# Kernel tuning notes

Measured on AMD Instinct MI355X. Metric: run time of the kernel, lower is better.

The kernel has to match this reference:

```python
import jax, jax.numpy as jnp
import numpy as np

# fp4 e2m1 positive value grid and midpoints between adjacent grid values
_GRID = jnp.array([0.0, 0.5, 1.0, 1.5, 2.0, 3.0, 4.0, 6.0], dtype=jnp.float32)
_MIDS = jnp.array([0.25, 0.75, 1.25, 1.75, 2.5, 3.5, 5.0], dtype=jnp.float32)
BLOCK = 32               # MX block size
E8M0_BIAS = 127
F32_MIN_NORMAL = float(2.0 ** -126)
F4_E2M1_MAX_POW2 = 2     # log2 of largest power-of-two <= 6.0 -> 4.0


def _quantize_fp4(a):
    """Round-to-nearest-even onto the signed e2m1 grid."""
    mag = jnp.clip(jnp.abs(a), 0.0, 6.0)
    idx = jnp.searchsorted(_MIDS, mag, side='left')  # ties round down
    mids_pad = jnp.concatenate([_MIDS, jnp.array([-1.0], jnp.float32)])
    tie = mag == mids_pad[idx]
    idx = jnp.where(tie & (idx % 2 == 1), idx + 1, idx)  # ties-to-even mantissa
    return _GRID[idx] * jnp.where(a < 0, -1.0, 1.0)


def _floor_log2(m):
    """Exact floor(log2(m)) for m > 0, with corrections for fp rounding of log2."""
    e = jnp.floor(jnp.log2(m))
    e = jnp.where(jnp.exp2(e) > m, e - 1.0, e)
    e = jnp.where(jnp.exp2(e + 1.0) <= m, e + 1.0, e)
    return e


def _qdq_mxfp4(x):
    """Quantize-dequantize x to MX fp4_e2m1, block 32, FLOOR scale mode (to_mx + to_dtype)."""
    shp = x.shape
    xb = x.reshape(-1, BLOCK)
    max_abs = jnp.max(jnp.abs(xb), axis=1)
    eps = F32_MIN_NORMAL * (max_abs == 0).astype(jnp.float32)
    pow2 = _floor_log2(max_abs + eps)
    e_unb = jnp.clip(pow2 - F4_E2M1_MAX_POW2, -float(E8M0_BIAS), float(E8M0_BIAS) + 1.0)
    scale = jnp.maximum(jnp.exp2(e_unb), F32_MIN_NORMAL)  # [nblk]
    q = _quantize_fp4(xb / scale[:, None])
    return (q * scale[:, None]).reshape(shp)


def _dequant_weight(weight_packed, weight_scale, out_f, in_f):
    """Unpack uint8-packed fp4 (low nibble first), apply e8m0 block scales."""
    p = weight_packed.astype(jnp.int32)
    low = p & 0xF
    high = (p >> 4) & 0xF
    nib = jnp.stack([low, high], axis=-1).reshape(out_f, in_f)  # interleave low,high
    vals = _GRID[nib & 7] * jnp.where((nib & 8) > 0, -1.0, 1.0)
    s = jnp.exp2(weight_scale.astype(jnp.float32) - E8M0_BIAS)  # get_fp_scale(e8m0)
    return (vals.reshape(-1, BLOCK) * s[:, None]).reshape(out_f, in_f)


def setup_inputs() -> dict:
    key = jax.random.key(0)
    k1, k2, k3 = jax.random.split(key, 3)
    M, IN, OUT = 4096, 4096, 4096
    x = jax.random.normal(k1, (M, IN), dtype=jnp.float32)
    weight_packed = jax.random.randint(k2, (OUT, IN // 2), 0, 256, dtype=jnp.int32)
    weight_scale = jax.random.randint(k3, (OUT * IN // BLOCK,), 0, 135, dtype=jnp.int32)
    return {"x": x, "weight_packed": weight_packed, "weight_scale": weight_scale}


def reference(x, weight_packed, weight_scale):
    out_f = weight_packed.shape[0]
    in_f = weight_packed.shape[1] * 2
    xq = _qdq_mxfp4(x)                                       # qdq_mxfp4(x)
    w_dq = _dequant_weight(weight_packed, weight_scale, out_f, in_f)
    return xq @ w_dq.T                                       # matmul(x, w_dq.t())
```

## Files before the change

### kernel.cpp

```cpp
#include <hip/hip_runtime.h>
#include <stdint.h>

typedef __attribute__((ext_vector_type(4)))  int   intx4;
typedef __attribute__((ext_vector_type(8)))  int   intx8;
typedef __attribute__((ext_vector_type(16))) float floatx16;

#define GLL16(gp, lp)                                                               \
    __builtin_amdgcn_global_load_lds((const __attribute__((address_space(1))) unsigned int*)(gp), \
                                     (__attribute__((address_space(3))) unsigned int*)(lp), 16, 0, 0)
#define GLL4(gp, lp)                                                                \
    __builtin_amdgcn_global_load_lds((const __attribute__((address_space(1))) unsigned int*)(gp), \
                                     (__attribute__((address_space(3))) unsigned int*)(lp), 4, 0, 0)

__device__ __forceinline__ uint32_t enc1(float xv, float inv) {
    float a = fminf(fabsf(xv) * inv, 6.0f);
    int e;
    if (a < 2.0f)      e = (int)rintf(a + a);
    else if (a < 4.0f) e = (int)rintf(a) + 2;
    else               e = (int)rintf(a * 0.5f) + 4;
    return (uint32_t)e | ((__float_as_uint(xv) >> 28) & 8u);
}

__global__ __launch_bounds__(256) void quant_x_kernel(const float* __restrict__ x,
                                                      uint32_t* __restrict__ xq,
                                                      uint8_t* __restrict__ xs) {
    const int gl = blockIdx.x * 256 + threadIdx.x;
    const float4 v = ((const float4*)x)[gl];
    float m = fmaxf(fmaxf(fabsf(v.x), fabsf(v.y)), fmaxf(fabsf(v.z), fabsf(v.w)));
    m = fmaxf(m, __shfl_xor(m, 1));
    m = fmaxf(m, __shfl_xor(m, 2));
    m = fmaxf(m, __shfl_xor(m, 4));
    const unsigned ef = __float_as_uint(m) >> 23;
    const unsigned code = (ef < 3u) ? 1u : (ef - 2u);
    const float inv = __uint_as_float((254u - code) << 23);
    const uint32_t p = enc1(v.x, inv)        | (enc1(v.y, inv) << 4)
                     | (enc1(v.z, inv) << 8) | (enc1(v.w, inv) << 12);
    ((uint16_t*)xq)[gl] = (uint16_t)p;
    if ((gl & 7) == 0) xs[gl >> 3] = (uint8_t)code;
}

__global__ __launch_bounds__(256) void repack_kernel(const int* __restrict__ wp,
                                                     uint32_t* __restrict__ wrep,
                                                     int n4w,
                                                     const int* __restrict__ wsc,
                                                     uint32_t* __restrict__ ws,
                                                     int n4s) {
    const int t = blockIdx.x * 256 + threadIdx.x;
    if (t < n4w) {
        const int4 p = ((const int4*)wp)[t];
        wrep[t] = (uint32_t)(p.x & 0xFF) | ((uint32_t)(p.y & 0xFF) << 8)
                | ((uint32_t)(p.z & 0xFF) << 16) | ((uint32_t)(p.w & 0xFF) << 24);
    } else if (t - n4w < n4s) {
        const int i = t - n4w;
        const int4 p = ((const int4*)wsc)[i];
        ws[i] = (uint32_t)(p.x & 0xFF) | ((uint32_t)(p.y & 0xFF) << 8)
              | ((uint32_t)(p.z & 0xFF) << 16) | ((uint32_t)(p.w & 0xFF) << 24);
    }
}

__global__ __launch_bounds__(256) void tpose_s_kernel(const uint8_t* __restrict__ nat,
                                                      uint8_t* __restrict__ xs_t,
                                                      uint8_t* __restrict__ ws_t,
                                                      int R, int Ck) {
    __shared__ uint8_t raw[128 * 32];
    const int r0 = blockIdx.x * 128;
    const int c0 = blockIdx.y * 32;
    const int t = threadIdx.x;
    {
        const int r = t >> 1, hf = t & 1;
        const uint4 v = *(const uint4*)(nat + (size_t)(r0 + r) * Ck + c0 + hf * 16);
        *(uint4*)(raw + r * 32 + hf * 16) = v;
    }
    __syncthreads();
    const int c = t >> 3, q = t & 7;
    uint32_t d[4];
#pragma unroll
    for (int j = 0; j < 4; ++j) {
        const int mb = q * 16 + j * 4;
        d[j] = (uint32_t)raw[(mb + 0) * 32 + c]
             | ((uint32_t)raw[(mb + 1) * 32 + c] << 8)
             | ((uint32_t)raw[(mb + 2) * 32 + c] << 16)
             | ((uint32_t)raw[(mb + 3) * 32 + c] << 24);
    }
    uint8_t* outp = (r0 < R) ? (xs_t + (size_t)(c0 + c) * R + r0)
                             : (ws_t + (size_t)(c0 + c) * R + (r0 - R));
    *(uint4*)(outp + q * 16) = make_uint4(d[0], d[1], d[2], d[3]);
}

__global__ __launch_bounds__(256) void gemm_mx_kernel(const uint8_t* __restrict__ Apk,
                                                      const uint8_t* __restrict__ Bpk,
                                                      const uint8_t* __restrict__ AsT,
                                                      const uint8_t* __restrict__ BsT,
                                                      float* __restrict__ C,
                                                      int M, int N, int K) {
    __shared__ __align__(16) uint8_t sA[8192];
    __shared__ __align__(16) uint8_t sB[8192];
    __shared__ __align__(16) uint8_t sS[1024];

    const int tid = threadIdx.x;
    const int bm0 = blockIdx.y << 7;
    const int bn0 = blockIdx.x << 7;
    const int wave = tid >> 6;
    const int lane = tid & 63;
    const int wm = (wave >> 1) << 6;
    const int wn = (wave & 1) << 6;
    const int row = lane & 31;
    const int h = lane >> 5;
    const int Kb = K >> 1;

    const int s0 = tid, s1 = tid + 256;
    const int r0 = s0 >> 2, p0 = (s0 & 3) ^ ((r0 >> 1) & 3);
    const int r1 = s1 >> 2, p1 = (s1 & 3) ^ ((r1 >> 1) & 3);
    const uint8_t* Ag0 = Apk + (size_t)(bm0 + r0) * Kb + p0 * 16;
    const uint8_t* Ag1 = Apk + (size_t)(bm0 + r1) * Kb + p1 * 16;
    const uint8_t* Bg0 = Bpk + (size_t)(bn0 + r0) * Kb + p0 * 16;
    const uint8_t* Bg1 = Bpk + (size_t)(bn0 + r1) * Kb + p1 * 16;

    const int st = tid & 127;
    const int sj = st >> 5, si = st & 31;
    const uint8_t* Sg = (tid < 128) ? (AsT + (size_t)sj * M + bm0 + si * 4)
                                    : (BsT + (size_t)sj * N + bn0 + si * 4);
    uint8_t* Sl = sS + ((tid < 128) ? 0 : 512) + st * 4;
    const size_t sAdv = (size_t)4 * (size_t)((tid < 128) ? M : N);

    floatx16 acc[2][2];
#pragma unroll
    for (int a = 0; a < 2; ++a)
#pragma unroll
        for (int b = 0; b < 2; ++b)
#pragma unroll
            for (int r = 0; r < 16; ++r) acc[a][b][r] = 0.f;

    const int nchunk = K >> 7;
    const int ar0 = wm + row, ar1 = wm + 32 + row;
    const int br0 = wn + row, br1 = wn + 32 + row;

    for (int c = 0; c < nchunk; ++c) {
        __syncthreads();
        const size_t koff = (size_t)c << 6;
        GLL16(Ag0 + koff, sA + s0 * 16);
        GLL16(Ag1 + koff, sA + s1 * 16);
        GLL16(Bg0 + koff, sB + s0 * 16);
        GLL16(Bg1 + koff, sB + s1 * 16);
        GLL4(Sg + (size_t)c * sAdv, Sl);
        __syncthreads();

#pragma unroll
        for (int s = 0; s < 2; ++s) {
            const int kp = 2 * s + h;
            intx4 a4[2], b4[2];
            int sa[2], sb[2];
            a4[0] = *(const intx4*)(sA + ar0 * 64 + ((kp ^ ((ar0 >> 1) & 3)) << 4));
            a4[1] = *(const intx4*)(sA + ar1 * 64 + ((kp ^ ((ar1 >> 1) & 3)) << 4));
            b4[0] = *(const intx4*)(sB + br0 * 64 + ((kp ^ ((br0 >> 1) & 3)) << 4));
            b4[1] = *(const intx4*)(sB + br1 * 64 + ((kp ^ ((br1 >> 1) & 3)) << 4));
            sa[0] = sS[kp * 128 + ar0];
            sa[1] = sS[kp * 128 + ar1];
            sb[0] = sS[512 + kp * 128 + br0];
            sb[1] = sS[512 + kp * 128 + br1];
#pragma unroll
            for (int mt = 0; mt < 2; ++mt)
#pragma unroll
                for (int nt = 0; nt < 2; ++nt) {
                    intx8 a8 = {a4[mt][0], a4[mt][1], a4[mt][2], a4[mt][3], 0, 0, 0, 0};
                    intx8 b8 = {b4[nt][0], b4[nt][1], b4[nt][2], b4[nt][3], 0, 0, 0, 0};
                    acc[mt][nt] = __builtin_amdgcn_mfma_scale_f32_32x32x64_f8f6f4(
                        a8, b8, acc[mt][nt], 4, 4, 0, sa[mt], 0, sb[nt]);
                }
        }
    }

#pragma unroll
    for (int mt = 0; mt < 2; ++mt)
#pragma unroll
        for (int nt = 0; nt < 2; ++nt) {
            const int col = bn0 + wn + nt * 32 + row;
#pragma unroll
            for (int g = 0; g < 4; ++g) {
                const int rw = bm0 + wm + mt * 32 + 8 * g + 4 * h;
#pragma unroll
                for (int q = 0; q < 4; ++q)
                    C[(size_t)(rw + q) * N + col] = acc[mt][nt][4 * g + q];
            }
        }
}

extern "C" void kernel_launch(void* const* d_in, const int* in_sizes, int n_in,
                              void* d_out, int out_size, void* d_ws, size_t ws_size,
                              hipStream_t stream) {
    const float* x = (const float*)d_in[0];
    const int* wp = (const int*)d_in[1];
    const int* wsc = (const int*)d_in[2];
    float* out = (float*)d_out;

    const int K = 4096;
    const int M = in_sizes[0] / K;
    const int N = (in_sizes[1] * 2) / K;
    const int kbpr = K / 32;
    const int npack = N * K / 2;

    uint32_t* xq   = (uint32_t*)d_ws;
    uint8_t*  xs   = (uint8_t*)d_ws + (size_t)M * K / 2;
    uint8_t*  ws   = xs + (size_t)M * kbpr;
    uint32_t* wrep = (uint32_t*)(ws + (size_t)N * kbpr);
    uint8_t*  xs_t = (uint8_t*)(wrep + (size_t)npack / 4);
    uint8_t*  ws_t = xs_t + (size_t)M * kbpr;

    const int n4w = npack / 4;
    const int n4s = (N * kbpr) / 4;

    quant_x_kernel<<<(M * K / 4) / 256, 256, 0, stream>>>(x, xq, xs);
    repack_kernel<<<(n4w + n4s + 255) / 256, 256, 0, stream>>>(wp, wrep, n4w,
                                                               wsc, (uint32_t*)ws, n4s);
    dim3 tg(2 * M / 128, kbpr / 32);
    tpose_s_kernel<<<tg, 256, 0, stream>>>(xs, xs_t, ws_t, M, kbpr);

    dim3 grid(N / 128, M / 128);
    gemm_mx_kernel<<<grid, 256, 0, stream>>>((const uint8_t*)xq, (const uint8_t*)wrep,
                                             xs_t, ws_t, out, M, N, K);
}
```

Measured before the change: 193.0 us.

## Triple-buffer LDS tiles in MX GEMM with async prefetch two chunks ahead

Replaces the single-buffered load-sync-compute loop with a three-stage LDS ring where global_load_lds for chunk c+2 is issued before computing chunk c. Explicit vmcnt waits let outstanding loads overlap MFMA work, hiding global memory latency that previously stalled each iteration. This triples LDS use per block, which may cut occupancy, and relies on hand-counted vmcnt values being correct.

```diff
diff --git a/kernel.cpp b/kernel.cpp
--- a/kernel.cpp
+++ b/kernel.cpp
@@ -93,9 +93,9 @@
                                                       const uint8_t* __restrict__ BsT,
                                                       float* __restrict__ C,
                                                       int M, int N, int K) {
-    __shared__ __align__(16) uint8_t sA[8192];
-    __shared__ __align__(16) uint8_t sB[8192];
-    __shared__ __align__(16) uint8_t sS[1024];
+    __shared__ __align__(16) uint8_t sA[3][8192];
+    __shared__ __align__(16) uint8_t sB[3][8192];
+    __shared__ __align__(16) uint8_t sS[3][1024];
 
     const int tid = threadIdx.x;
     const int bm0 = blockIdx.y << 7;
@@ -120,7 +120,7 @@
     const int sj = st >> 5, si = st & 31;
     const uint8_t* Sg = (tid < 128) ? (AsT + (size_t)sj * M + bm0 + si * 4)
                                     : (BsT + (size_t)sj * N + bn0 + si * 4);
-    uint8_t* Sl = sS + ((tid < 128) ? 0 : 512) + st * 4;
+    const int sloff = ((tid < 128) ? 0 : 512) + st * 4;
     const size_t sAdv = (size_t)4 * (size_t)((tid < 128) ? M : N);
 
     floatx16 acc[2][2];
@@ -135,29 +135,32 @@
     const int ar0 = wm + row, ar1 = wm + 32 + row;
     const int br0 = wn + row, br1 = wn + 32 + row;
 
-    for (int c = 0; c < nchunk; ++c) {
-        __syncthreads();
+    auto STAGE = [&](int bf, int c) {
         const size_t koff = (size_t)c << 6;
-        GLL16(Ag0 + koff, sA + s0 * 16);
-        GLL16(Ag1 + koff, sA + s1 * 16);
-        GLL16(Bg0 + koff, sB + s0 * 16);
-        GLL16(Bg1 + koff, sB + s1 * 16);
-        GLL4(Sg + (size_t)c * sAdv, Sl);
-        __syncthreads();
-
+        GLL16(Ag0 + koff, &sA[bf][s0 * 16]);
+        GLL16(Ag1 + koff, &sA[bf][s1 * 16]);
+        GLL16(Bg0 + koff, &sB[bf][s0 * 16]);
+        GLL16(Bg1 + koff, &sB[bf][s1 * 16]);
+        GLL4(Sg + (size_t)c * sAdv, &sS[bf][sloff]);
+    };
+
+    auto COMPUTE = [&](int bf) {
+        const uint8_t* cA = sA[bf];
+        const uint8_t* cB = sB[bf];
+        const uint8_t* cS = sS[bf];
 #pragma unroll
         for (int s = 0; s < 2; ++s) {
             const int kp = 2 * s + h;
             intx4 a4[2], b4[2];
             int sa[2], sb[2];
-            a4[0] = *(const intx4*)(sA + ar0 * 64 + ((kp ^ ((ar0 >> 1) & 3)) << 4));
-            a4[1] = *(const intx4*)(sA + ar1 * 64 + ((kp ^ ((ar1 >> 1) & 3)) << 4));
-            b4[0] = *(const intx4*)(sB + br0 * 64 + ((kp ^ ((br0 >> 1) & 3)) << 4));
-            b4[1] = *(const intx4*)(sB + br1 * 64 + ((kp ^ ((br1 >> 1) & 3)) << 4));
-            sa[0] = sS[kp * 128 + ar0];
-            sa[1] = sS[kp * 128 + ar1];
-            sb[0] = sS[512 + kp * 128 + br0];
-            sb[1] = sS[512 + kp * 128 + br1];
+            a4[0] = *(const intx4*)(cA + ar0 * 64 + ((kp ^ ((ar0 >> 1) & 3)) << 4));
+            a4[1] = *(const intx4*)(cA + ar1 * 64 + ((kp ^ ((ar1 >> 1) & 3)) << 4));
+            b4[0] = *(const intx4*)(cB + br0 * 64 + ((kp ^ ((br0 >> 1) & 3)) << 4));
+            b4[1] = *(const intx4*)(cB + br1 * 64 + ((kp ^ ((br1 >> 1) & 3)) << 4));
+            sa[0] = cS[kp * 128 + ar0];
+            sa[1] = cS[kp * 128 + ar1];
+            sb[0] = cS[512 + kp * 128 + br0];
+            sb[1] = cS[512 + kp * 128 + br1];
 #pragma unroll
             for (int mt = 0; mt < 2; ++mt)
 #pragma unroll
@@ -168,6 +171,23 @@
                         a8, b8, acc[mt][nt], 4, 4, 0, sa[mt], 0, sb[nt]);
                 }
         }
+    };
+
+    STAGE(0, 0);
+    STAGE(1, 1);
+
+    int i0 = 0, i1 = 1, i2 = 2;
+    for (int c = 0; c < nchunk; ++c) {
+        __builtin_amdgcn_s_barrier();
+        asm volatile("" ::: "memory");
+        if (c + 2 < nchunk) STAGE(i2, c + 2);
+        if (c < nchunk - 2)      asm volatile("s_waitcnt vmcnt(10)" ::: "memory");
+        else if (c == nchunk - 2) asm volatile("s_waitcnt vmcnt(5)" ::: "memory");
+        else                      asm volatile("s_waitcnt vmcnt(0)" ::: "memory");
+        __builtin_amdgcn_s_barrier();
+        asm volatile("" ::: "memory");
+        COMPUTE(i0);
+        const int t = i0; i0 = i1; i1 = i2; i2 = t;
     }
 
 #pragma unroll
```

New measurement: 201.8 us. 1.05x slower.

## Double the K-chunk per iteration in MX fp4 GEMM with wider swizzle

Applied to the files above, without the earlier changes.

Each main-loop iteration of the GEMM now stages 256 K elements instead of 128, doubling the shared tiles for A, B and the scales and running four MFMA sub-steps per chunk. The LDS row stride grows to 128 bytes with an 8-way XOR swizzle to avoid bank conflicts. The aim is to halve the number of barrier pairs and make each load burst larger. The cost is doubled shared memory per block, which may lower occupancy, and there is still no double buffering.

```diff
diff --git a/kernel.cpp b/kernel.cpp
--- a/kernel.cpp
+++ b/kernel.cpp
@@ -93,9 +93,9 @@
                                                       const uint8_t* __restrict__ BsT,
                                                       float* __restrict__ C,
                                                       int M, int N, int K) {
-    __shared__ __align__(16) uint8_t sA[8192];
-    __shared__ __align__(16) uint8_t sB[8192];
-    __shared__ __align__(16) uint8_t sS[1024];
+    __shared__ __align__(16) uint8_t sA[16384];
+    __shared__ __align__(16) uint8_t sB[16384];
+    __shared__ __align__(16) uint8_t sS[2048];
 
     const int tid = threadIdx.x;
     const int bm0 = blockIdx.y << 7;
@@ -108,20 +108,25 @@
     const int h = lane >> 5;
     const int Kb = K >> 1;
 
-    const int s0 = tid, s1 = tid + 256;
-    const int r0 = s0 >> 2, p0 = (s0 & 3) ^ ((r0 >> 1) & 3);
-    const int r1 = s1 >> 2, p1 = (s1 & 3) ^ ((r1 >> 1) & 3);
-    const uint8_t* Ag0 = Apk + (size_t)(bm0 + r0) * Kb + p0 * 16;
-    const uint8_t* Ag1 = Apk + (size_t)(bm0 + r1) * Kb + p1 * 16;
-    const uint8_t* Bg0 = Bpk + (size_t)(bn0 + r0) * Kb + p0 * 16;
-    const uint8_t* Bg1 = Bpk + (size_t)(bn0 + r1) * Kb + p1 * 16;
+    const uint8_t* Ag[4];
+    const uint8_t* Bg[4];
+#pragma unroll
+    for (int i = 0; i < 4; ++i) {
+        const int s = tid + 256 * i;
+        const int r = s >> 3;
+        const int p = (s & 7) ^ (r & 7);
+        Ag[i] = Apk + (size_t)(bm0 + r) * Kb + p * 16;
+        Bg[i] = Bpk + (size_t)(bn0 + r) * Kb + p * 16;
+    }
 
     const int st = tid & 127;
     const int sj = st >> 5, si = st & 31;
-    const uint8_t* Sg = (tid < 128) ? (AsT + (size_t)sj * M + bm0 + si * 4)
-                                    : (BsT + (size_t)sj * N + bn0 + si * 4);
-    uint8_t* Sl = sS + ((tid < 128) ? 0 : 512) + st * 4;
-    const size_t sAdv = (size_t)4 * (size_t)((tid < 128) ? M : N);
+    const size_t sR = (size_t)((tid < 128) ? M : N);
+    const uint8_t* Sg1 = ((tid < 128) ? (AsT + (size_t)sj * M + bm0)
+                                      : (BsT + (size_t)sj * N + bn0)) + si * 4;
+    const uint8_t* Sg2 = Sg1 + 4 * sR;
+    const size_t sAdv = 8 * sR;
+    const int soff = ((tid < 128) ? 0 : 1024) + st * 4;
 
     floatx16 acc[2][2];
 #pragma unroll
@@ -131,33 +136,34 @@
 #pragma unroll
             for (int r = 0; r < 16; ++r) acc[a][b][r] = 0.f;
 
-    const int nchunk = K >> 7;
+    const int nchunk = K >> 8;
     const int ar0 = wm + row, ar1 = wm + 32 + row;
     const int br0 = wn + row, br1 = wn + 32 + row;
 
     for (int c = 0; c < nchunk; ++c) {
         __syncthreads();
-        const size_t koff = (size_t)c << 6;
-        GLL16(Ag0 + koff, sA + s0 * 16);
-        GLL16(Ag1 + koff, sA + s1 * 16);
-        GLL16(Bg0 + koff, sB + s0 * 16);
-        GLL16(Bg1 + koff, sB + s1 * 16);
-        GLL4(Sg + (size_t)c * sAdv, Sl);
+        const size_t koff = (size_t)c << 7;
+#pragma unroll
+        for (int i = 0; i < 4; ++i) GLL16(Ag[i] + koff, sA + (tid + 256 * i) * 16);
+#pragma unroll
+        for (int i = 0; i < 4; ++i) GLL16(Bg[i] + koff, sB + (tid + 256 * i) * 16);
+        GLL4(Sg1 + (size_t)c * sAdv, sS + soff);
+        GLL4(Sg2 + (size_t)c * sAdv, sS + soff + 512);
         __syncthreads();
 
 #pragma unroll
-        for (int s = 0; s < 2; ++s) {
+        for (int s = 0; s < 4; ++s) {
             const int kp = 2 * s + h;
             intx4 a4[2], b4[2];
             int sa[2], sb[2];
-            a4[0] = *(const intx4*)(sA + ar0 * 64 + ((kp ^ ((ar0 >> 1) & 3)) << 4));
-            a4[1] = *(const intx4*)(sA + ar1 * 64 + ((kp ^ ((ar1 >> 1) & 3)) << 4));
-            b4[0] = *(const intx4*)(sB + br0 * 64 + ((kp ^ ((br0 >> 1) & 3)) << 4));
-            b4[1] = *(const intx4*)(sB + br1 * 64 + ((kp ^ ((br1 >> 1) & 3)) << 4));
+            a4[0] = *(const intx4*)(sA + ar0 * 128 + ((kp ^ (ar0 & 7)) << 4));
+            a4[1] = *(const intx4*)(sA + ar1 * 128 + ((kp ^ (ar1 & 7)) << 4));
+            b4[0] = *(const intx4*)(sB + br0 * 128 + ((kp ^ (br0 & 7)) << 4));
+            b4[1] = *(const intx4*)(sB + br1 * 128 + ((kp ^ (br1 & 7)) << 4));
             sa[0] = sS[kp * 128 + ar0];
             sa[1] = sS[kp * 128 + ar1];
-            sb[0] = sS[512 + kp * 128 + br0];
-            sb[1] = sS[512 + kp * 128 + br1];
+            sb[0] = sS[1024 + kp * 128 + br0];
+            sb[1] = sS[1024 + kp * 128 + br1];
 #pragma unroll
             for (int mt = 0; mt < 2; ++mt)
 #pragma unroll
```

New measurement: 192.3 us. Within noise of the previous version (-0.4%).
